# Kernel tuning notes

Hardware: AMD Instinct MI355X
Metric: run time of the kernel (lower is better)

The kernel has to match this reference:

```python
import jax, jax.numpy as jnp
import numpy as np

BETA = 0.9
THRESH = 1.0
SLOPE = 25.0  # fast_sigmoid surrogate slope

@jax.custom_vjp
def spike(x):
    # forward: heaviside(mem - threshold); backward: fast-sigmoid surrogate
    return (x > 0).astype(x.dtype)

def _spike_fwd(x):
    return (x > 0).astype(x.dtype), x

def _spike_bwd(x, g):
    return (g / (SLOPE * jnp.abs(x) + 1.0) ** 2,)

spike.defvjp(_spike_fwd, _spike_bwd)

def lif_step(mem, cur):
    # snntorch Leaky, reset_mechanism='subtract': reset from previous mem (detached)
    reset = jax.lax.stop_gradient((mem > THRESH).astype(cur.dtype))
    mem_new = BETA * mem + cur - reset * THRESH
    spk = spike(mem_new - THRESH)
    return spk, mem_new

def setup_inputs() -> dict:
    key = jax.random.key(0)
    ks = jax.random.split(key, 10)
    B, S, T = 256, 8, 25
    A, V, H, E = 512, 512, 256, 128
    a_seq = (jax.random.uniform(ks[0], (B, S, T, A)) < 0.2).astype(jnp.float32)
    v_seq = (jax.random.uniform(ks[1], (B, S, T, V)) < 0.2).astype(jnp.float32)
    def lin(kw, kb, out_d, in_d):
        lim = 1.0 / np.sqrt(in_d)
        W = jax.random.uniform(kw, (out_d, in_d), minval=-lim, maxval=lim, dtype=jnp.float32)
        b = jax.random.uniform(kb, (out_d,), minval=-lim, maxval=lim, dtype=jnp.float32)
        return W, b
    W_a1, b_a1 = lin(ks[2], ks[3], H, A)
    W_a2, b_a2 = lin(ks[4], ks[5], E, H)
    W_v1, b_v1 = lin(ks[6], ks[7], H, V)
    W_v2, b_v2 = lin(ks[8], ks[9], E, H)
    return dict(a_seq=a_seq, v_seq=v_seq, W_a1=W_a1, b_a1=b_a1, W_a2=W_a2, b_a2=b_a2,
                W_v1=W_v1, b_v1=b_v1, W_v2=W_v2, b_v2=b_v2)

def reference(a_seq, v_seq, W_a1, b_a1, W_a2, b_a2, W_v1, b_v1, W_v2, b_v2):
    B, S, T, A = a_seq.shape
    V = v_seq.shape[-1]
    H = W_a1.shape[0]
    E = W_a2.shape[0]
    BS = B * S  # segments are independent -> fold into batch
    a = a_seq.reshape(BS, T, A).transpose(1, 0, 2)  # [T, BS, A]
    v = v_seq.reshape(BS, T, V).transpose(1, 0, 2)  # [T, BS, V]

    def step(carry, xs):
        ma1, ma2, mv1, mv2, _, _ = carry
        at, vt = xs
        spk_a1, ma1 = lif_step(ma1, at @ W_a1.T + b_a1)
        spk_a2, ma2 = lif_step(ma2, spk_a1 @ W_a2.T + b_a2)
        spk_v1, mv1 = lif_step(mv1, vt @ W_v1.T + b_v1)
        spk_v2, mv2 = lif_step(mv2, spk_v1 @ W_v2.T + b_v2)
        return (ma1, ma2, mv1, mv2, spk_a2, spk_v2), None

    z = jnp.zeros
    init = (z((BS, H)), z((BS, E)), z((BS, H)), z((BS, E)), z((BS, E)), z((BS, E)))
    (ma1, ma2, mv1, mv2, spk_a2, spk_v2), _ = jax.lax.scan(step, init, (a, v))
    combined = jnp.concatenate([spk_a2, spk_v2], axis=1)  # [BS, 2E]
    norm = jnp.linalg.norm(combined, axis=1, keepdims=True)
    combined = combined / jnp.maximum(norm, 1e-12)  # F.normalize p=2 dim=1
    embs = combined.reshape(B, S, 2 * E)
    return embs.mean(axis=1)  # [B, 2E]
```

## Files before the change

kernel.cpp:

```cpp
#include <hip/hip_runtime.h>


typedef short bf16x8 __attribute__((ext_vector_type(8)));
typedef float f32x4 __attribute__((ext_vector_type(4)));

#define RBIG 51200

__device__ __forceinline__ void glds16(const void* g, void* l) {
    __builtin_amdgcn_global_load_lds((const __attribute__((address_space(1))) void*)g,
                                     (__attribute__((address_space(3))) void*)l, 16, 0, 0);
}

__global__ void prep_w(const float* __restrict__ Wa1, const float* __restrict__ Wv1,
                       const float* __restrict__ Wa2, const float* __restrict__ Wv2,
                       unsigned short* __restrict__ W1s, unsigned short* __restrict__ W2s) {
    int idx = blockIdx.x * 256 + threadIdx.x;
    float w;
    unsigned short* dst;
    int K, k;
    if (idx < 262144) {
        int p = idx >> 17, rem = idx & 131071;
        int n = rem >> 9; k = rem & 511; K = 512;
        const float* src = p ? Wv1 : Wa1;
        w = src[(size_t)n * 512 + k];
        dst = W1s + (size_t)p * 256 * 1536 + (size_t)n * 1536;
    } else {
        int j = idx - 262144;
        int p = j >> 15, rem = j & 32767;
        int n = rem >> 8; k = rem & 255; K = 256;
        const float* src = p ? Wv2 : Wa2;
        w = src[(size_t)n * 256 + k];
        dst = W2s + (size_t)p * 128 * 768 + (size_t)n * 768;
    }
    unsigned int u  = __float_as_uint(w);
    unsigned int hi = u & 0xFFFF0000u;
    float r1 = w - __uint_as_float(hi);
    unsigned int mi = __float_as_uint(r1) & 0xFFFF0000u;
    float r2 = r1 - __uint_as_float(mi);
    dst[k]         = (unsigned short)(hi >> 16);
    dst[K + k]     = (unsigned short)(mi >> 16);
    dst[2 * K + k] = (unsigned short)(__float_as_uint(r2) >> 16);
}

template <int KSRC, int NT, int BM, int BN, int MINW, bool AF32>
__global__ __launch_bounds__(256, MINW) void gemmS(
    const void* __restrict__ A0, const void* __restrict__ A1,
    const unsigned short* __restrict__ Ws, float* __restrict__ C) {
    constexpr int KE   = 3 * KSRC;
    constexpr int NKB  = KSRC / 64;
    constexpr int MFR  = BM / 2 / 16;
    constexpr int NFR  = BN / 2 / 16;
    constexpr int AESZ = AF32 ? 4 : 2;
    constexpr int NBY  = NT / BN;
    constexpr int NAG  = BM * 64 * AESZ / 16 / 256;
    constexpr int NBG  = BN * 64 * 2 / 16 / 256;
    constexpr int GPRA = 64 * AESZ / 16;

    __shared__ __align__(1024) char Al[BM * 64 * AESZ];
    __shared__ __align__(1024) unsigned short Bl[BN * 64];

    const int tid  = threadIdx.x, lane = tid & 63, wave = tid >> 6;
    const int wm   = wave >> 1, wn = wave & 1;

    const int nwg = gridDim.x;
    const int orig = blockIdx.x;
    const int lid = (orig & 7) * (nwg >> 3) + (orig >> 3);
    const int by = lid % NBY;
    const int t0 = lid / NBY;
    const int bz = t0 & 1;
    const int bx = t0 >> 1;
    const size_t row0 = (size_t)bx * BM;

    const char* Abase = (const char*)(bz ? A1 : A0) + row0 * KSRC * AESZ;
    const char* Bbase = (const char*)Ws + ((size_t)bz * NT + (size_t)by * BN) * KE * 2;

    const int rowA0 = tid / GPRA, slA = tid % GPRA;
    const size_t offA0 = (size_t)rowA0 * KSRC * AESZ + (size_t)((slA ^ (rowA0 & 7)) << 4);
    const int rowB0 = tid >> 3, slB = tid & 7;
    const size_t offB0 = (size_t)rowB0 * KE * 2 + (size_t)((slB ^ (rowB0 & 7)) << 4);
    const int dst0 = wave * 1024;

    auto stageA = [&](int kb) {
        const char* s = Abase + (size_t)kb * 64 * AESZ + offA0;
        char* d = Al + dst0;
#pragma unroll
        for (int j = 0; j < NAG; ++j)
            glds16(s + (size_t)j * (64 * KSRC), d + j * 4096);
    };
    auto stageB = [&](int kb, int sp) {
        const char* s = Bbase + ((size_t)sp * KSRC + (size_t)kb * 64) * 2 + offB0;
        char* d = (char*)Bl + dst0;
#pragma unroll
        for (int j = 0; j < NBG; ++j)
            glds16(s + (size_t)j * (64 * KE), d + j * 4096);
    };

    f32x4 acc[MFR][NFR];
    f32x4 zz = {0.f, 0.f, 0.f, 0.f};
#pragma unroll
    for (int i = 0; i < MFR; ++i)
#pragma unroll
        for (int j = 0; j < NFR; ++j) acc[i][j] = zz;

    const int rfr = lane & 15;
    for (int kb = 0; kb < NKB; ++kb) {
#pragma unroll 1
        for (int s = 0; s < 3; ++s) {
            if (s == 0) stageA(kb);
            stageB(kb, s);
            __syncthreads();
#pragma unroll
            for (int ks = 0; ks < 2; ++ks) {
                const int kbase = ks * 32 + ((lane >> 4) << 3);
                bf16x8 bb[NFR];
#pragma unroll
                for (int ni = 0; ni < NFR; ++ni) {
                    int n = wn * (BN / 2) + ni * 16 + rfr;
                    bb[ni] = *(const bf16x8*)&Bl[(n * 64 + kbase) ^ ((n & 7) << 3)];
                }
#pragma unroll
                for (int mi = 0; mi < MFR; ++mi) {
                    int r = wm * (BM / 2) + mi * 16 + rfr;
                    bf16x8 av;
                    if constexpr (AF32) {
                        const float* Af = (const float*)Al;
                        int e1 = (r * 64 + kbase) ^ ((r & 7) << 2);
                        uint4 ua = *(const uint4*)&Af[e1];
                        uint4 ub = *(const uint4*)&Af[e1 ^ 4];
                        uint4 w;
                        w.x = (ua.y & 0xFFFF0000u) | (ua.x >> 16);
                        w.y = (ua.w & 0xFFFF0000u) | (ua.z >> 16);
                        w.z = (ub.y & 0xFFFF0000u) | (ub.x >> 16);
                        w.w = (ub.w & 0xFFFF0000u) | (ub.z >> 16);
                        av = __builtin_bit_cast(bf16x8, w);
                    } else {
                        const unsigned short* Au = (const unsigned short*)Al;
                        av = *(const bf16x8*)&Au[(r * 64 + kbase) ^ ((r & 7) << 3)];
                    }
#pragma unroll
                    for (int ni = 0; ni < NFR; ++ni)
                        acc[mi][ni] = __builtin_amdgcn_mfma_f32_16x16x32_bf16(
                            av, bb[ni], acc[mi][ni], 0, 0, 0);
                }
            }
            __syncthreads();
        }
    }

    float* Cp = C + (size_t)bz * RBIG * NT;
    int r4 = ((lane >> 4) << 2), cl = lane & 15;
#pragma unroll
    for (int mi = 0; mi < MFR; ++mi)
#pragma unroll
        for (int ni = 0; ni < NFR; ++ni) {
            size_t col = (size_t)by * BN + wn * (BN / 2) + ni * 16 + cl;
#pragma unroll
            for (int j = 0; j < 4; ++j) {
                size_t row = row0 + wm * (BM / 2) + mi * 16 + r4 + j;
                Cp[row * NT + col] = acc[mi][ni][j];
            }
        }
}

__global__ void lif1_k(const float* __restrict__ cur, const float* __restrict__ ba1,
                       const float* __restrict__ bv1, unsigned int* __restrict__ spk) {
    int r = blockIdx.x, p = blockIdx.y, d = threadIdx.x;
    const float* c0 = cur + ((size_t)p * RBIG + (size_t)r * 25) * 256 + 2 * d;
    const float* bias = p ? bv1 : ba1;
    float b0 = bias[2 * d], b1 = bias[2 * d + 1];
    float2 cv[25];
#pragma unroll
    for (int t = 0; t < 25; ++t) cv[t] = *(const float2*)(c0 + (size_t)t * 256);
    unsigned int* sp = spk + ((size_t)p * RBIG + (size_t)r * 25) * 128 + d;
    float m0 = 0.f, m1 = 0.f;
#pragma unroll
    for (int t = 0; t < 25; ++t) {
        float r0 = (m0 > 1.f) ? 1.f : 0.f;
        float r1 = (m1 > 1.f) ? 1.f : 0.f;
        m0 = 0.9f * m0 + (cv[t].x + b0) - r0;
        m1 = 0.9f * m1 + (cv[t].y + b1) - r1;
        unsigned int w = (m0 > 1.f ? 0x3F80u : 0u) | (m1 > 1.f ? 0x3F800000u : 0u);
        sp[(size_t)t * 128] = w;
    }
}

__global__ void tail_k(const float* __restrict__ cur2, const float* __restrict__ ba2,
                       const float* __restrict__ bv2, float* __restrict__ out) {
    int b = blockIdx.x, d = threadIdx.x;
    int p = d >> 7, e = d & 127;
    const float* bias = p ? bv2 : ba2;
    float bo = bias[e];
    __shared__ float part[4];
    float acc = 0.f;
    for (int s = 0; s < 8; ++s) {
        int r = b * 8 + s;
        const float* c0 = cur2 + ((size_t)p * RBIG + (size_t)r * 25) * 128 + e;
        float cv[25];
#pragma unroll
        for (int t = 0; t < 25; ++t) cv[t] = c0[(size_t)t * 128];
        float m = 0.f;
#pragma unroll
        for (int t = 0; t < 25; ++t) {
            float rs = (m > 1.f) ? 1.f : 0.f;
            m = 0.9f * m + (cv[t] + bo) - rs;
        }
        float v = (m > 1.f) ? 1.f : 0.f;
        float sq = v;
#pragma unroll
        for (int off = 32; off > 0; off >>= 1) sq += __shfl_down(sq, off);
        if ((d & 63) == 0) part[d >> 6] = sq;
        __syncthreads();
        float nrm = sqrtf(part[0] + part[1] + part[2] + part[3]);
        acc += v / fmaxf(nrm, 1e-12f);
        __syncthreads();
    }
    out[(size_t)b * 256 + d] = acc * 0.125f;
}

extern "C" void kernel_launch(void* const* d_in, const int* in_sizes, int n_in,
                              void* d_out, int out_size, void* d_ws, size_t ws_size,
                              hipStream_t stream) {
    const float* a_seq = (const float*)d_in[0];
    const float* v_seq = (const float*)d_in[1];
    const float* W_a1  = (const float*)d_in[2];
    const float* b_a1  = (const float*)d_in[3];
    const float* W_a2  = (const float*)d_in[4];
    const float* b_a2  = (const float*)d_in[5];
    const float* W_v1  = (const float*)d_in[6];
    const float* b_v1  = (const float*)d_in[7];
    const float* W_v2  = (const float*)d_in[8];
    const float* b_v2  = (const float*)d_in[9];

    char* ws = (char*)d_ws;
    unsigned short* W1s  = (unsigned short*)(ws);
    unsigned short* W2s  = (unsigned short*)(ws + 1572864);
    unsigned short* spk1 = (unsigned short*)(ws + 1966080);
    float*          curb = (float*)(ws + 54394880);
    float*          out  = (float*)d_out;

    prep_w<<<1280, 256, 0, stream>>>(W_a1, W_v1, W_a2, W_v2, W1s, W2s);

    gemmS<512, 256, 128, 128, 3, true><<<1600, 256, 0, stream>>>(
        a_seq, v_seq, W1s, curb);
    lif1_k<<<dim3(2048, 2), 128, 0, stream>>>(curb, b_a1, b_v1, (unsigned int*)spk1);

    gemmS<256, 128, 64, 128, 4, false><<<1600, 256, 0, stream>>>(
        spk1, spk1 + (size_t)RBIG * 256, W2s, curb);

    tail_k<<<256, 256, 0, stream>>>(curb, b_a2, b_v2, out);
}
```

Before: 363.3 us.

## Double-buffer weight tiles, prepack A to bf16 in LDS, split tail kernel

The GEMM kernel now double-buffers the weight-split tiles in LDS. Each K block's A fragments are loaded into registers once and reused across the three bf16 weight splits, so a stage's global loads overlap the previous stage's MFMAs. For the fp32 first-layer input, A is loaded into registers and converted to bf16 before being written to LDS, which halves A's LDS footprint and removes per-fragment conversion. The tail kernel is split into a per-segment kernel with 2048 blocks that normalizes and writes to scratch, plus a small mean kernel, to raise parallelism. The cost is more registers, one extra launch and an intermediate buffer round trip.

```diff
diff --git a/kernel.cpp b/kernel.cpp
--- a/kernel.cpp
+++ b/kernel.cpp
@@ -9,6 +9,9 @@
 __device__ __forceinline__ void glds16(const void* g, void* l) {
     __builtin_amdgcn_global_load_lds((const __attribute__((address_space(1))) void*)g,
                                      (__attribute__((address_space(3))) void*)l, 16, 0, 0);
+}
+__device__ __forceinline__ unsigned int pk2(float lo, float hi) {
+    return (__float_as_uint(hi) & 0xFFFF0000u) | (__float_as_uint(lo) >> 16);
 }
 
 __global__ void prep_w(const float* __restrict__ Wa1, const float* __restrict__ Wv1,
@@ -43,21 +46,19 @@
 }
 
 template <int KSRC, int NT, int BM, int BN, int MINW, bool AF32>
-__global__ __launch_bounds__(256, MINW) void gemmS(
+__global__ __launch_bounds__(256, MINW) void gemmT(
     const void* __restrict__ A0, const void* __restrict__ A1,
     const unsigned short* __restrict__ Ws, float* __restrict__ C) {
     constexpr int KE   = 3 * KSRC;
     constexpr int NKB  = KSRC / 64;
     constexpr int MFR  = BM / 2 / 16;
     constexpr int NFR  = BN / 2 / 16;
-    constexpr int AESZ = AF32 ? 4 : 2;
     constexpr int NBY  = NT / BN;
-    constexpr int NAG  = BM * 64 * AESZ / 16 / 256;
-    constexpr int NBG  = BN * 64 * 2 / 16 / 256;
-    constexpr int GPRA = 64 * AESZ / 16;
-
-    __shared__ __align__(1024) char Al[BM * 64 * AESZ];
-    __shared__ __align__(1024) unsigned short Bl[BN * 64];
+    constexpr int NBG  = BN / 32;
+    constexpr int NAGL = BM / 32;
+
+    __shared__ __align__(1024) unsigned short Al[BM * 64];
+    __shared__ __align__(1024) unsigned short Bl[2][BN * 64];
 
     const int tid  = threadIdx.x, lane = tid & 63, wave = tid >> 6;
     const int wm   = wave >> 1, wn = wave & 1;
@@ -71,28 +72,44 @@
     const int bx = t0 >> 1;
     const size_t row0 = (size_t)bx * BM;
 
-    const char* Abase = (const char*)(bz ? A1 : A0) + row0 * KSRC * AESZ;
+    const char* Abase = (const char*)(bz ? A1 : A0) + row0 * KSRC * (AF32 ? 4 : 2);
     const char* Bbase = (const char*)Ws + ((size_t)bz * NT + (size_t)by * BN) * KE * 2;
 
-    const int rowA0 = tid / GPRA, slA = tid % GPRA;
-    const size_t offA0 = (size_t)rowA0 * KSRC * AESZ + (size_t)((slA ^ (rowA0 & 7)) << 4);
     const int rowB0 = tid >> 3, slB = tid & 7;
     const size_t offB0 = (size_t)rowB0 * KE * 2 + (size_t)((slB ^ (rowB0 & 7)) << 4);
     const int dst0 = wave * 1024;
-
-    auto stageA = [&](int kb) {
-        const char* s = Abase + (size_t)kb * 64 * AESZ + offA0;
-        char* d = Al + dst0;
-#pragma unroll
-        for (int j = 0; j < NAG; ++j)
-            glds16(s + (size_t)j * (64 * KSRC), d + j * 4096);
-    };
-    auto stageB = [&](int kb, int sp) {
+    auto stageB = [&](int kb, int sp, int buf) {
         const char* s = Bbase + ((size_t)sp * KSRC + (size_t)kb * 64) * 2 + offB0;
-        char* d = (char*)Bl + dst0;
+        char* d = (char*)Bl[buf] + dst0;
 #pragma unroll
         for (int j = 0; j < NBG; ++j)
-            glds16(s + (size_t)j * (64 * KE), d + j * 4096);
+            glds16(s + (size_t)j * (32 * KE * 2), d + j * 4096);
+    };
+
+    const int rowA = tid >> 1, halfA = tid & 1;
+    auto loadAh = [&](int kb, int hv, float4 (&a)[4]) {
+        const float* p = (const float*)Abase + (size_t)rowA * KSRC + kb * 64 + halfA * 32 + hv * 16;
+#pragma unroll
+        for (int q = 0; q < 4; ++q) a[q] = *(const float4*)(p + q * 4);
+    };
+    auto packwA = [&](int hv, float4 (&a)[4]) {
+        uint4 u0, u1;
+        u0.x = pk2(a[0].x, a[0].y); u0.y = pk2(a[0].z, a[0].w);
+        u0.z = pk2(a[1].x, a[1].y); u0.w = pk2(a[1].z, a[1].w);
+        u1.x = pk2(a[2].x, a[2].y); u1.y = pk2(a[2].z, a[2].w);
+        u1.z = pk2(a[3].x, a[3].y); u1.w = pk2(a[3].z, a[3].w);
+        int g0 = halfA * 4 + hv * 2;
+        *(uint4*)&Al[rowA * 64 + ((g0 ^ (rowA & 7)) << 3)]       = u0;
+        *(uint4*)&Al[rowA * 64 + (((g0 + 1) ^ (rowA & 7)) << 3)] = u1;
+    };
+    const int rowAS = tid >> 3, slAS = tid & 7;
+    const size_t offA0 = (size_t)rowAS * KSRC * 2 + (size_t)((slAS ^ (rowAS & 7)) << 4);
+    auto stageA_lds = [&](int kb) {
+        const char* s = Abase + (size_t)kb * 64 * 2 + offA0;
+        char* d = (char*)Al + dst0;
+#pragma unroll
+        for (int j = 0; j < NAGL; ++j)
+            glds16(s + (size_t)j * (32 * KSRC * 2), d + j * 4096);
     };
 
     f32x4 acc[MFR][NFR];
@@ -102,49 +119,69 @@
 #pragma unroll
         for (int j = 0; j < NFR; ++j) acc[i][j] = zz;
 
+    const int ko0 = (lane >> 4) << 3;
     const int rfr = lane & 15;
+    bf16x8 af[MFR][2];
+
+    auto loadAfrags = [&]() {
+#pragma unroll
+        for (int mi = 0; mi < MFR; ++mi)
+#pragma unroll
+            for (int ks = 0; ks < 2; ++ks) {
+                int r = wm * (BM / 2) + mi * 16 + rfr;
+                af[mi][ks] = *(const bf16x8*)&Al[(r * 64 + ks * 32 + ko0) ^ ((r & 7) << 3)];
+            }
+    };
+    auto comp = [&](int buf) {
+#pragma unroll
+        for (int ks = 0; ks < 2; ++ks) {
+            const int kbase = ks * 32 + ko0;
+            bf16x8 bb[NFR];
+#pragma unroll
+            for (int ni = 0; ni < NFR; ++ni) {
+                int n = wn * (BN / 2) + ni * 16 + rfr;
+                bb[ni] = *(const bf16x8*)&Bl[buf][(n * 64 + kbase) ^ ((n & 7) << 3)];
+            }
+#pragma unroll
+            for (int mi = 0; mi < MFR; ++mi)
+#pragma unroll
+                for (int ni = 0; ni < NFR; ++ni)
+                    acc[mi][ni] = __builtin_amdgcn_mfma_f32_16x16x32_bf16(
+                        af[mi][ks], bb[ni], acc[mi][ni], 0, 0, 0);
+        }
+    };
+
+    float4 a0h[4], a1h[4];
+    if constexpr (AF32) {
+        loadAh(0, 0, a0h); loadAh(0, 1, a1h);
+        packwA(0, a0h);    packwA(1, a1h);
+    } else {
+        stageA_lds(0);
+    }
+    stageB(0, 0, 0);
+    __syncthreads();
+
+#pragma unroll 1
     for (int kb = 0; kb < NKB; ++kb) {
-#pragma unroll 1
-        for (int s = 0; s < 3; ++s) {
-            if (s == 0) stageA(kb);
-            stageB(kb, s);
-            __syncthreads();
-#pragma unroll
-            for (int ks = 0; ks < 2; ++ks) {
-                const int kbase = ks * 32 + ((lane >> 4) << 3);
-                bf16x8 bb[NFR];
-#pragma unroll
-                for (int ni = 0; ni < NFR; ++ni) {
-                    int n = wn * (BN / 2) + ni * 16 + rfr;
-                    bb[ni] = *(const bf16x8*)&Bl[(n * 64 + kbase) ^ ((n & 7) << 3)];
-                }
-#pragma unroll
-                for (int mi = 0; mi < MFR; ++mi) {
-                    int r = wm * (BM / 2) + mi * 16 + rfr;
-                    bf16x8 av;
-                    if constexpr (AF32) {
-                        const float* Af = (const float*)Al;
-                        int e1 = (r * 64 + kbase) ^ ((r & 7) << 2);
-                        uint4 ua = *(const uint4*)&Af[e1];
-                        uint4 ub = *(const uint4*)&Af[e1 ^ 4];
-                        uint4 w;
-                        w.x = (ua.y & 0xFFFF0000u) | (ua.x >> 16);
-                        w.y = (ua.w & 0xFFFF0000u) | (ua.z >> 16);
-                        w.z = (ub.y & 0xFFFF0000u) | (ub.x >> 16);
-                        w.w = (ub.w & 0xFFFF0000u) | (ub.z >> 16);
-                        av = __builtin_bit_cast(bf16x8, w);
-                    } else {
-                        const unsigned short* Au = (const unsigned short*)Al;
-                        av = *(const bf16x8*)&Au[(r * 64 + kbase) ^ ((r & 7) << 3)];
-                    }
-#pragma unroll
-                    for (int ni = 0; ni < NFR; ++ni)
-                        acc[mi][ni] = __builtin_amdgcn_mfma_f32_16x16x32_bf16(
-                            av, bb[ni], acc[mi][ni], 0, 0, 0);
-                }
-            }
-            __syncthreads();
+        const bool more = (kb + 1 < NKB);
+        const int pb = kb & 1, qb = pb ^ 1;
+        loadAfrags();
+        stageB(kb, 1, qb);
+        if constexpr (AF32) { if (more) loadAh(kb + 1, 0, a0h); }
+        comp(pb);
+        __syncthreads();
+        stageB(kb, 2, pb);
+        if constexpr (AF32) {
+            if (more) { packwA(0, a0h); loadAh(kb + 1, 1, a1h); }
+        } else {
+            if (more) stageA_lds(kb + 1);
         }
+        comp(qb);
+        __syncthreads();
+        if (more) stageB(kb + 1, 0, qb);
+        if constexpr (AF32) { if (more) packwA(1, a1h); }
+        comp(pb);
+        __syncthreads();
     }
 
     float* Cp = C + (size_t)bz * RBIG * NT;
@@ -184,36 +221,38 @@
     }
 }
 
-__global__ void tail_k(const float* __restrict__ cur2, const float* __restrict__ ba2,
-                       const float* __restrict__ bv2, float* __restrict__ out) {
-    int b = blockIdx.x, d = threadIdx.x;
+__global__ void tail1_k(const float* __restrict__ cur2, const float* __restrict__ ba2,
+                        const float* __restrict__ bv2, float* __restrict__ normd) {
+    int r = blockIdx.x, d = threadIdx.x;
     int p = d >> 7, e = d & 127;
     const float* bias = p ? bv2 : ba2;
     float bo = bias[e];
+    const float* c0 = cur2 + ((size_t)p * RBIG + (size_t)r * 25) * 128 + e;
+    float cv[25];
+#pragma unroll
+    for (int t = 0; t < 25; ++t) cv[t] = c0[(size_t)t * 128];
+    float m = 0.f;
+#pragma unroll
+    for (int t = 0; t < 25; ++t) {
+        float rs = (m > 1.f) ? 1.f : 0.f;
+        m = 0.9f * m + (cv[t] + bo) - rs;
+    }
+    float v = (m > 1.f) ? 1.f : 0.f;
     __shared__ float part[4];
+    float sq = v;
+#pragma unroll
+    for (int off = 32; off > 0; off >>= 1) sq += __shfl_down(sq, off);
+    if ((d & 63) == 0) part[d >> 6] = sq;
+    __syncthreads();
+    float nrm = sqrtf(part[0] + part[1] + part[2] + part[3]);
+    normd[(size_t)r * 256 + d] = v / fmaxf(nrm, 1e-12f);
+}
+
+__global__ void tail2_k(const float* __restrict__ normd, float* __restrict__ out) {
+    int b = blockIdx.x, d = threadIdx.x;
     float acc = 0.f;
-    for (int s = 0; s < 8; ++s) {
-        int r = b * 8 + s;
-        const float* c0 = cur2 + ((size_t)p * RBIG + (size_t)r * 25) * 128 + e;
-        float cv[25];
-#pragma unroll
-        for (int t = 0; t < 25; ++t) cv[t] = c0[(size_t)t * 128];
-        float m = 0.f;
-#pragma unroll
-        for (int t = 0; t < 25; ++t) {
-            float rs = (m > 1.f) ? 1.f : 0.f;
-            m = 0.9f * m + (cv[t] + bo) - rs;
-        }
-        float v = (m > 1.f) ? 1.f : 0.f;
-        float sq = v;
-#pragma unroll
-        for (int off = 32; off > 0; off >>= 1) sq += __shfl_down(sq, off);
-        if ((d & 63) == 0) part[d >> 6] = sq;
-        __syncthreads();
-        float nrm = sqrtf(part[0] + part[1] + part[2] + part[3]);
-        acc += v / fmaxf(nrm, 1e-12f);
-        __syncthreads();
-    }
+#pragma unroll
+    for (int s = 0; s < 8; ++s) acc += normd[((size_t)(b * 8 + s)) * 256 + d];
     out[(size_t)b * 256 + d] = acc * 0.125f;
 }
 
@@ -236,16 +275,18 @@
     unsigned short* W2s  = (unsigned short*)(ws + 1572864);
     unsigned short* spk1 = (unsigned short*)(ws + 1966080);
     float*          curb = (float*)(ws + 54394880);
+    float*          normd= (float*)(ws + 1966080);
     float*          out  = (float*)d_out;
 
     prep_w<<<1280, 256, 0, stream>>>(W_a1, W_v1, W_a2, W_v2, W1s, W2s);
 
-    gemmS<512, 256, 128, 128, 3, true><<<1600, 256, 0, stream>>>(
+    gemmT<512, 256, 128, 128, 3, true><<<1600, 256, 0, stream>>>(
         a_seq, v_seq, W1s, curb);
     lif1_k<<<dim3(2048, 2), 128, 0, stream>>>(curb, b_a1, b_v1, (unsigned int*)spk1);
 
-    gemmS<256, 128, 64, 128, 4, false><<<1600, 256, 0, stream>>>(
+    gemmT<256, 128, 64, 128, 4, false><<<1600, 256, 0, stream>>>(
         spk1, spk1 + (size_t)RBIG * 256, W2s, curb);
 
-    tail_k<<<256, 256, 0, stream>>>(curb, b_a2, b_v2, out);
-}
+    tail1_k<<<2048, 256, 0, stream>>>(curb, b_a2, b_v2, normd);
+    tail2_k<<<256, 256, 0, stream>>>(normd, out);
+}
```

Result: slower. 608.4 us (+67.5%).
